# Kernel optimization log

Hardware: AMD Instinct MI355X
Metric: run time of the kernel (lower is better)

The kernel has to match this reference:

```python
import jax, jax.numpy as jnp
import numpy as np

NUM_HEADS = 8

def setup_inputs() -> dict:
    key = jax.random.key(0)
    ks = jax.random.split(key, 12)
    T, B, C, D = 2048, 4, 512, 512
    s = 1.0 / np.sqrt(C)
    return {
        "key_in": jax.random.normal(ks[0], (T, B, C), jnp.float32),
        "value_in": jax.random.normal(ks[1], (T, B, C), jnp.float32),
        "query_in": jax.random.normal(ks[2], (T, B, C), jnp.float32),
        "Wk": jax.random.normal(ks[3], (C, D), jnp.float32) * s,
        "bk": jax.random.normal(ks[4], (D,), jnp.float32) * 0.01,
        "Wv": jax.random.normal(ks[5], (C, D), jnp.float32) * s,
        "bv": jax.random.normal(ks[6], (D,), jnp.float32) * 0.01,
        "Wq": jax.random.normal(ks[7], (C, D), jnp.float32) * s,
        "bq": jax.random.normal(ks[8], (D,), jnp.float32) * 0.01,
        "Wo": jax.random.normal(ks[9], (D, D), jnp.float32) * (1.0 / np.sqrt(D)),
        "bo": jax.random.normal(ks[10], (D,), jnp.float32) * 0.01,
    }

def reference(key_in, value_in, query_in, Wk, bk, Wv, bv, Wq, bq, Wo, bo):
    T, B, C = query_in.shape
    D = Wq.shape[1]
    H = NUM_HEADS
    hd = D // H
    scale = 1.0 / np.sqrt(hd).astype(np.float32)
    # Linear projections on (T, B, C) -> (T, B, D), then the original's
    # row-major view(B, -1, H, hd) followed by transpose(1, 2) -> (B, H, T, hd)
    def proj(x, W, b):
        y = x @ W + b                      # (T, B, D)
        return y.reshape(B, -1, H, hd).transpose(0, 2, 1, 3)  # (B, H, T, hd)
    q = proj(query_in, Wq, bq)
    k = proj(key_in, Wk, bk)
    v = proj(value_in, Wv, bv)
    scores = jnp.einsum("bhqd,bhkd->bhqk", q, k) * scale  # (B, H, T, T)
    attn = jax.nn.softmax(scores, axis=-1)
    x = jnp.einsum("bhqk,bhkd->bhqd", attn, v)            # (B, H, T, hd)
    x = x.transpose(0, 2, 1, 3).reshape(T, B, D)          # matches .view(T, B, d_model)
    return x @ Wo + bo
```

## Files before the change

### kernel.cpp

```cpp
#include <hip/hip_runtime.h>
#include <math.h>

#define MROWS 8192
#define DM    512
#define SEQL  2048
#define HDIM  64

typedef __attribute__((ext_vector_type(4))) float floatx4;
typedef _Float16 half2v __attribute__((ext_vector_type(2)));
typedef _Float16 half4v __attribute__((ext_vector_type(4)));
typedef _Float16 half8v __attribute__((ext_vector_type(8)));

#define CEXP 0.18033688011f

__device__ __forceinline__ void gll16(const void* g, void* l) {
    __builtin_amdgcn_global_load_lds(
        (const __attribute__((address_space(1))) unsigned int*)g,
        (__attribute__((address_space(3))) unsigned int*)l, 16, 0, 0);
}

__device__ __forceinline__ half4v pack4(float a, float b, float c, float d) {
    half2v lo = __builtin_bit_cast(half2v, __builtin_amdgcn_cvt_pkrtz(a, b));
    half2v hi = __builtin_bit_cast(half2v, __builtin_amdgcn_cvt_pkrtz(c, d));
    half4v r;
    r[0] = lo[0]; r[1] = lo[1]; r[2] = hi[0]; r[3] = hi[1];
    return r;
}

__global__ __launch_bounds__(256) void cast3(const float* __restrict__ s0,
                                             const float* __restrict__ s1,
                                             const float* __restrict__ s2,
                                             _Float16* __restrict__ d0,
                                             _Float16* __restrict__ d1,
                                             _Float16* __restrict__ d2) {
    const float* s = blockIdx.z == 0 ? s0 : (blockIdx.z == 1 ? s1 : s2);
    _Float16* d = blockIdx.z == 0 ? d0 : (blockIdx.z == 1 ? d1 : d2);
    const size_t i = ((size_t)blockIdx.x * 256 + threadIdx.x) * 8;
    const float4 f0 = *(const float4*)&s[i];
    const float4 f1 = *(const float4*)&s[i + 4];
    half8v o;
    o[0] = (_Float16)f0.x; o[1] = (_Float16)f0.y; o[2] = (_Float16)f0.z; o[3] = (_Float16)f0.w;
    o[4] = (_Float16)f1.x; o[5] = (_Float16)f1.y; o[6] = (_Float16)f1.z; o[7] = (_Float16)f1.w;
    *(half8v*)&d[i] = o;
}

__global__ __launch_bounds__(256) void transw(const float* __restrict__ w0,
                                              const float* __restrict__ w1,
                                              const float* __restrict__ w2,
                                              const float* __restrict__ w3,
                                              _Float16* __restrict__ t0,
                                              _Float16* __restrict__ t1,
                                              _Float16* __restrict__ t2,
                                              _Float16* __restrict__ t3) {
    __shared__ float tile[32][33];
    const float* W = blockIdx.z == 0 ? w0 : (blockIdx.z == 1 ? w1 : (blockIdx.z == 2 ? w2 : w3));
    _Float16* T = blockIdx.z == 0 ? t0 : (blockIdx.z == 1 ? t1 : (blockIdx.z == 2 ? t2 : t3));
    const float sc = (blockIdx.z == 0) ? CEXP : 1.0f;
    const int tx = threadIdx.x & 31, ty = threadIdx.x >> 5;
    const int x = blockIdx.x * 32 + tx;
    const int y0 = blockIdx.y * 32;
#pragma unroll
    for (int i = 0; i < 4; ++i)
        tile[ty + i * 8][tx] = W[(size_t)(y0 + ty + i * 8) * DM + x];
    __syncthreads();
    const int xo = y0 + tx;
#pragma unroll
    for (int i = 0; i < 4; ++i)
        T[(size_t)(blockIdx.x * 32 + ty + i * 8) * DM + xo] = (_Float16)(tile[tx][ty + i * 8] * sc);
}

__global__ __launch_bounds__(256, 3) void gemm_f16(
        const _Float16* __restrict__ A0, const _Float16* __restrict__ A1, const _Float16* __restrict__ A2,
        const _Float16* __restrict__ B0, const _Float16* __restrict__ B1, const _Float16* __restrict__ B2,
        const float* __restrict__ c0, const float* __restrict__ c1, const float* __restrict__ c2,
        void* __restrict__ o0, void* __restrict__ o1, void* __restrict__ o2,
        int modes, float bscale0) {
    __shared__ _Float16 As[128 * 64];
    __shared__ _Float16 Bs[64 * 64];
    const int z = blockIdx.z;
    const _Float16* A  = z == 0 ? A0 : (z == 1 ? A1 : A2);
    const _Float16* Bt = z == 0 ? B0 : (z == 1 ? B1 : B2);
    const float* bias  = z == 0 ? c0 : (z == 1 ? c1 : c2);
    void* outp         = z == 0 ? o0 : (z == 1 ? o1 : o2);
    const int mode = (modes >> (z * 4)) & 15;
    const float bscale = (z == 0) ? bscale0 : 1.0f;

    const int tid = threadIdx.x;
    const int w = tid >> 6;
    const int l15 = tid & 15, quad = (tid & 63) >> 4;
    const int n0 = blockIdx.x * 64, m0 = blockIdx.y * 128;

    floatx4 acc[2][4];
#pragma unroll
    for (int i = 0; i < 2; ++i)
#pragma unroll
        for (int j = 0; j < 4; ++j) acc[i][j] = (floatx4){0.f, 0.f, 0.f, 0.f};

    for (int kt = 0; kt < DM / 64; ++kt) {
        __syncthreads();
#pragma unroll
        for (int i = 0; i < 4; ++i) {
            const int c = i * 256 + tid;
            const int row = c >> 3, g = c & 7;
            const int kg = g ^ (row & 7);
            gll16(&A[(size_t)(m0 + row) * DM + kt * 64 + kg * 8], &As[c * 8]);
        }
#pragma unroll
        for (int i = 0; i < 2; ++i) {
            const int c = i * 256 + tid;
            const int row = c >> 3, g = c & 7;
            const int kg = g ^ (row & 7);
            gll16(&Bt[(size_t)(n0 + row) * DM + kt * 64 + kg * 8], &Bs[c * 8]);
        }
        __syncthreads();
#pragma unroll
        for (int ks = 0; ks < 2; ++ks) {
            half8v af[2], bfr[4];
#pragma unroll
            for (int i = 0; i < 2; ++i) {
                const int row = w * 32 + i * 16 + l15;
                af[i] = *(const half8v*)&As[row * 64 + ((ks * 4 + quad) ^ (row & 7)) * 8];
            }
#pragma unroll
            for (int j = 0; j < 4; ++j) {
                const int row = j * 16 + l15;
                bfr[j] = *(const half8v*)&Bs[row * 64 + ((ks * 4 + quad) ^ (row & 7)) * 8];
            }
#pragma unroll
            for (int i = 0; i < 2; ++i)
#pragma unroll
                for (int j = 0; j < 4; ++j)
                    acc[i][j] = __builtin_amdgcn_mfma_f32_16x16x32_f16(af[i], bfr[j], acc[i][j], 0, 0, 0);
        }
    }
#pragma unroll
    for (int j = 0; j < 4; ++j) {
        const int col = n0 + j * 16 + l15;
        const float bv = bias[col] * bscale;
#pragma unroll
        for (int i = 0; i < 2; ++i) {
            const int rb = m0 + w * 32 + i * 16 + quad * 4;
            if (mode == 2) {
                float* of = (float*)outp;
#pragma unroll
                for (int r = 0; r < 4; ++r)
                    of[(size_t)(rb + r) * DM + col] = acc[i][j][r] + bv;
            } else if (mode == 0) {
                _Float16* oh = (_Float16*)outp;
#pragma unroll
                for (int r = 0; r < 4; ++r)
                    oh[(size_t)(rb + r) * DM + col] = (_Float16)(acc[i][j][r] + bv);
            } else {
                _Float16* oh = (_Float16*)outp;
                const int g = rb >> 11, seq = rb & 2047;
                half4v pv;
#pragma unroll
                for (int r = 0; r < 4; ++r) pv[r] = (_Float16)(acc[i][j][r] + bv);
                *(half4v*)&oh[((size_t)g * DM + col) * SEQL + seq] = pv;
            }
        }
    }
}

__global__ __launch_bounds__(256, 2) void attn_mfma(const _Float16* __restrict__ Q16,
                                                    const _Float16* __restrict__ K16,
                                                    const _Float16* __restrict__ Vt,
                                                    _Float16* __restrict__ O16) {
    __shared__ _Float16 Ks[2][64 * 64];
    __shared__ _Float16 Vs[2][64 * 64];

    const int tid  = threadIdx.x;
    const int lane = tid & 63;
    const int l15  = lane & 15;
    const int quad = lane >> 4;

    const int pair = blockIdx.y;
    const int grp  = pair >> 3;
    const int h    = pair & 7;
    const int q0   = blockIdx.x * 128;
    const int rQ   = grp * SEQL + q0 + (tid >> 6) * 32;
    const int cb   = h * HDIM;

    const _Float16* Kbase = K16 + (size_t)grp * SEQL * DM + cb;
    const _Float16* Vbase = Vt + (size_t)grp * DM * SEQL + (size_t)cb * SEQL;

    half8v qf[2][2];
#pragma unroll
    for (int qt = 0; qt < 2; ++qt)
#pragma unroll
        for (int ks = 0; ks < 2; ++ks)
            qf[qt][ks] = *(const half8v*)&Q16[(size_t)(rQ + qt * 16 + l15) * DM + cb + ks * 32 + quad * 8];

    floatx4 oacc[2][4], lacc[2];
#pragma unroll
    for (int qt = 0; qt < 2; ++qt) {
        lacc[qt] = (floatx4){0.f, 0.f, 0.f, 0.f};
#pragma unroll
        for (int dt = 0; dt < 4; ++dt) oacc[qt][dt] = (floatx4){0.f, 0.f, 0.f, 0.f};
    }
    half4v ones;
    ones[0] = (_Float16)1.f; ones[1] = (_Float16)1.f; ones[2] = (_Float16)1.f; ones[3] = (_Float16)1.f;

    const int cK = tid * 2;

#define STAGE(KT, B)                                                            \
    {                                                                           \
        _Float16* ksb = &Ks[B][0];                                              \
        _Float16* vsb = &Vs[B][0];                                              \
        _Pragma("unroll")                                                       \
        for (int i_ = 0; i_ < 4; ++i_) {                                        \
            const int c_ = i_ * 256 + tid;                                      \
            if (c_ < 512) {                                                     \
                const int key_ = c_ >> 3, g_ = c_ & 7;                          \
                const int dg_ = g_ ^ (key_ & 7);                                \
                gll16(&Kbase[(size_t)((KT) * 64 + key_) * DM + dg_ * 8],        \
                      &ksb[c_ * 8]);                                            \
            } else {                                                            \
                const int cv_ = c_ - 512;                                       \
                const int d_ = cv_ >> 3, g_ = cv_ & 7;                          \
                const int kg_ = g_ ^ (d_ & 7);                                  \
                gll16(&Vbase[(size_t)d_ * SEQL + (KT) * 64 + kg_ * 8],          \
                      &vsb[cv_ * 8]);                                           \
            }                                                                   \
        }                                                                       \
    }

    STAGE(0, 0)

    for (int kt = 0; kt < SEQL / 64; ++kt) {
        const int cur = kt & 1;
        __syncthreads();
        if (kt + 1 < SEQL / 64) STAGE(kt + 1, cur ^ 1)

        const _Float16* ksb = &Ks[cur][0];
        const _Float16* vsb = &Vs[cur][0];

        floatx4 st[4][2];
#pragma unroll
        for (int ktile = 0; ktile < 4; ++ktile) {
            const int key = ktile * 16 + l15;
            const half8v kf0 = *(const half8v*)&ksb[key * 64 + ((0 + quad) ^ (key & 7)) * 8];
            const half8v kf1 = *(const half8v*)&ksb[key * 64 + ((4 + quad) ^ (key & 7)) * 8];
#pragma unroll
            for (int qt = 0; qt < 2; ++qt) {
                floatx4 z = {0.f, 0.f, 0.f, 0.f};
                z = __builtin_amdgcn_mfma_f32_16x16x32_f16(kf0, qf[qt][0], z, 0, 0, 0);
                st[ktile][qt] = __builtin_amdgcn_mfma_f32_16x16x32_f16(kf1, qf[qt][1], z, 0, 0, 0);
            }
        }

        half4v pa[4][2];
#pragma unroll
        for (int ktile = 0; ktile < 4; ++ktile)
#pragma unroll
            for (int qt = 0; qt < 2; ++qt)
                pa[ktile][qt] = pack4(__builtin_amdgcn_exp2f(st[ktile][qt][0]),
                                      __builtin_amdgcn_exp2f(st[ktile][qt][1]),
                                      __builtin_amdgcn_exp2f(st[ktile][qt][2]),
                                      __builtin_amdgcn_exp2f(st[ktile][qt][3]));

#pragma unroll
        for (int qt = 0; qt < 2; ++qt)
#pragma unroll
            for (int ktile = 0; ktile < 4; ++ktile)
                lacc[qt] = __builtin_amdgcn_mfma_f32_16x16x16f16(pa[ktile][qt], ones, lacc[qt], 0, 0, 0);

#pragma unroll
        for (int dt = 0; dt < 4; ++dt) {
            const int d = dt * 16 + l15;
#pragma unroll
            for (int ktile = 0; ktile < 4; ++ktile) {
                const int G = ktile * 2 + (quad >> 1);
                const int slot = G ^ (d & 7);
                const half4v vf = *(const half4v*)&vsb[d * 64 + slot * 8 + (quad & 1) * 4];
#pragma unroll
                for (int qt = 0; qt < 2; ++qt)
                    oacc[qt][dt] = __builtin_amdgcn_mfma_f32_16x16x16f16(pa[ktile][qt], vf, oacc[qt][dt], 0, 0, 0);
            }
        }
    }

#pragma unroll
    for (int qt = 0; qt < 2; ++qt)
#pragma unroll
        for (int r = 0; r < 4; ++r) {
            const float inv = __builtin_amdgcn_rcpf(lacc[qt][r]);
            const size_t rowoff = (size_t)(rQ + qt * 16 + quad * 4 + r) * DM + cb;
#pragma unroll
            for (int dt = 0; dt < 4; ++dt)
                O16[rowoff + dt * 16 + l15] = (_Float16)(oacc[qt][dt][r] * inv);
        }
}

extern "C" void kernel_launch(void* const* d_in, const int* in_sizes, int n_in,
                              void* d_out, int out_size, void* d_ws, size_t ws_size,
                              hipStream_t stream) {
    const float* key_in   = (const float*)d_in[0];
    const float* value_in = (const float*)d_in[1];
    const float* query_in = (const float*)d_in[2];
    const float* Wk = (const float*)d_in[3];
    const float* bk = (const float*)d_in[4];
    const float* Wv = (const float*)d_in[5];
    const float* bv = (const float*)d_in[6];
    const float* Wq = (const float*)d_in[7];
    const float* bq = (const float*)d_in[8];
    const float* Wo = (const float*)d_in[9];
    const float* bo = (const float*)d_in[10];
    float* out = (float*)d_out;

    const size_t MAT = (size_t)MROWS * DM;
    _Float16* Xq16 = (_Float16*)d_ws;
    _Float16* Xk16 = Xq16 + MAT;
    _Float16* Xv16 = Xk16 + MAT;
    _Float16* Q16  = Xv16 + MAT;
    _Float16* K16  = Q16 + MAT;
    _Float16* Vtb  = K16 + MAT;
    _Float16* Wqt  = Vtb + MAT;
    _Float16* Wkt  = Wqt + DM * DM;
    _Float16* Wvt  = Wkt + DM * DM;
    _Float16* Wot  = Wvt + DM * DM;
    _Float16* O16  = Xq16;

    const dim3 blk(256);

    cast3<<<dim3(2048, 1, 3), blk, 0, stream>>>(query_in, key_in, value_in, Xq16, Xk16, Xv16);
    transw<<<dim3(16, 16, 4), blk, 0, stream>>>(Wq, Wk, Wv, Wo, Wqt, Wkt, Wvt, Wot);

    gemm_f16<<<dim3(DM / 64, MROWS / 128, 3), blk, 0, stream>>>(
        Xq16, Xk16, Xv16, Wqt, Wkt, Wvt, bq, bk, bv,
        (void*)Q16, (void*)K16, (void*)Vtb, 0 | (0 << 4) | (1 << 8), CEXP);

    attn_mfma<<<dim3(SEQL / 128, 32), blk, 0, stream>>>(Q16, K16, Vtb, O16);

    gemm_f16<<<dim3(DM / 64, MROWS / 128, 1), blk, 0, stream>>>(
        O16, O16, O16, Wot, Wot, Wot, bo, bo, bo,
        (void*)out, (void*)out, (void*)out, 2, 1.0f);
}
```

Measured before the change: 206.5 us.

## Split attention over key range and add a combine kernel

The attention kernel now splits the key/value sequence into two halves along a new grid dimension. Each half writes unnormalized partial outputs and row sums to workspace, and a new combine kernel adds the halves and normalizes them. The aim is to double the number of blocks and raise the occupancy target to 4, so more waves are available to hide latency. In exchange there is an extra kernel launch and extra global memory traffic for the partials, and the tighter register budget may cause spills.

```diff
diff --git a/kernel.cpp b/kernel.cpp
--- a/kernel.cpp
+++ b/kernel.cpp
@@ -5,6 +5,7 @@
 #define DM    512
 #define SEQL  2048
 #define HDIM  64
+#define NSPLIT 2
 
 typedef __attribute__((ext_vector_type(4))) float floatx4;
 typedef _Float16 half2v __attribute__((ext_vector_type(2)));
@@ -162,10 +163,11 @@
     }
 }
 
-__global__ __launch_bounds__(256, 2) void attn_mfma(const _Float16* __restrict__ Q16,
+__global__ __launch_bounds__(256, 4) void attn_mfma(const _Float16* __restrict__ Q16,
                                                     const _Float16* __restrict__ K16,
                                                     const _Float16* __restrict__ Vt,
-                                                    _Float16* __restrict__ O16) {
+                                                    _Float16* __restrict__ Opart,
+                                                    float* __restrict__ lpart) {
     __shared__ _Float16 Ks[2][64 * 64];
     __shared__ _Float16 Vs[2][64 * 64];
 
@@ -174,12 +176,15 @@
     const int l15  = lane & 15;
     const int quad = lane >> 4;
 
-    const int pair = blockIdx.y;
-    const int grp  = pair >> 3;
-    const int h    = pair & 7;
-    const int q0   = blockIdx.x * 128;
-    const int rQ   = grp * SEQL + q0 + (tid >> 6) * 32;
-    const int cb   = h * HDIM;
+    const int pair  = blockIdx.y;
+    const int split = blockIdx.z;
+    const int grp   = pair >> 3;
+    const int h     = pair & 7;
+    const int q0    = blockIdx.x * 128;
+    const int rQ    = grp * SEQL + q0 + (tid >> 6) * 32;
+    const int cb    = h * HDIM;
+    const int NIT   = (SEQL / 64) / NSPLIT;
+    const int kt0   = split * NIT;
 
     const _Float16* Kbase = K16 + (size_t)grp * SEQL * DM + cb;
     const _Float16* Vbase = Vt + (size_t)grp * DM * SEQL + (size_t)cb * SEQL;
@@ -200,8 +205,6 @@
     }
     half4v ones;
     ones[0] = (_Float16)1.f; ones[1] = (_Float16)1.f; ones[2] = (_Float16)1.f; ones[3] = (_Float16)1.f;
-
-    const int cK = tid * 2;
 
 #define STAGE(KT, B)                                                            \
     {                                                                           \
@@ -225,12 +228,12 @@
         }                                                                       \
     }
 
-    STAGE(0, 0)
-
-    for (int kt = 0; kt < SEQL / 64; ++kt) {
-        const int cur = kt & 1;
+    STAGE(kt0, 0)
+
+    for (int it = 0; it < NIT; ++it) {
+        const int cur = it & 1;
         __syncthreads();
-        if (kt + 1 < SEQL / 64) STAGE(kt + 1, cur ^ 1)
+        if (it + 1 < NIT) STAGE(kt0 + it + 1, cur ^ 1)
 
         const _Float16* ksb = &Ks[cur][0];
         const _Float16* vsb = &Vs[cur][0];
@@ -280,16 +283,37 @@
         }
     }
 
+    _Float16* Op = Opart + (size_t)split * MROWS * DM;
 #pragma unroll
     for (int qt = 0; qt < 2; ++qt)
 #pragma unroll
         for (int r = 0; r < 4; ++r) {
-            const float inv = __builtin_amdgcn_rcpf(lacc[qt][r]);
-            const size_t rowoff = (size_t)(rQ + qt * 16 + quad * 4 + r) * DM + cb;
+            const int qrow = rQ + qt * 16 + quad * 4 + r;
+            const size_t rowoff = (size_t)qrow * DM + cb;
 #pragma unroll
             for (int dt = 0; dt < 4; ++dt)
-                O16[rowoff + dt * 16 + l15] = (_Float16)(oacc[qt][dt][r] * inv);
-        }
+                Op[rowoff + dt * 16 + l15] = (_Float16)oacc[qt][dt][r];
+            if (l15 == 0)
+                lpart[((size_t)split * MROWS + qrow) * 8 + h] = lacc[qt][r];
+        }
+}
+
+__global__ __launch_bounds__(256) void combine(const _Float16* __restrict__ Opart,
+                                               const float* __restrict__ lpart,
+                                               _Float16* __restrict__ O16) {
+    const size_t idx = (size_t)blockIdx.x * 256 + threadIdx.x;
+    const int row = idx >> 6;
+    const int c8 = (idx & 63) * 8;
+    const int h = c8 >> 6;
+    const float l = lpart[(size_t)row * 8 + h] + lpart[((size_t)MROWS + row) * 8 + h];
+    const float inv = 1.0f / l;
+    const half8v a = *(const half8v*)&Opart[(size_t)row * DM + c8];
+    const half8v b = *(const half8v*)&Opart[(size_t)MROWS * DM + (size_t)row * DM + c8];
+    half8v o;
+#pragma unroll
+    for (int i = 0; i < 8; ++i)
+        o[i] = (_Float16)(((float)a[i] + (float)b[i]) * inv);
+    *(half8v*)&O16[(size_t)row * DM + c8] = o;
 }
 
 extern "C" void kernel_launch(void* const* d_in, const int* in_sizes, int n_in,
@@ -319,7 +343,9 @@
     _Float16* Wkt  = Wqt + DM * DM;
     _Float16* Wvt  = Wkt + DM * DM;
     _Float16* Wot  = Wvt + DM * DM;
-    _Float16* O16  = Xq16;
+    float*    lpart = (float*)(Wot + DM * DM);
+    _Float16* Opart = Xq16;
+    _Float16* O16   = Xv16;
 
     const dim3 blk(256);
 
@@ -330,7 +356,8 @@
         Xq16, Xk16, Xv16, Wqt, Wkt, Wvt, bq, bk, bv,
         (void*)Q16, (void*)K16, (void*)Vtb, 0 | (0 << 4) | (1 << 8), CEXP);
 
-    attn_mfma<<<dim3(SEQL / 128, 32), blk, 0, stream>>>(Q16, K16, Vtb, O16);
+    attn_mfma<<<dim3(SEQL / 128, 32, NSPLIT), blk, 0, stream>>>(Q16, K16, Vtb, Opart, lpart);
+    combine<<<dim3(MROWS * DM / 8 / 256), blk, 0, stream>>>(Opart, lpart, O16);
 
     gemm_f16<<<dim3(DM / 64, MROWS / 128, 1), blk, 0, stream>>>(
         O16, O16, O16, Wot, Wot, Wot, bo, bo, bo,
```

Result: slower. 213.6 us (+3.4%).
